# Kernel tuning notes

Measured on AMD Instinct MI355X. Metric: run time of the kernel, lower is better.

Reference implementation:

```python
import jax, jax.numpy as jnp
import numpy as np

N_NODES = 100000
N_EDGES = 1600000


def gcn_conv(x, edge_index, W, b):
    # PyG GCNConv: add self-loops, symmetric degree normalization,
    # linear transform, scatter-sum aggregation, + bias.
    n = x.shape[0]
    loop = jnp.arange(n, dtype=edge_index.dtype)
    src = jnp.concatenate([edge_index[0], loop])
    dst = jnp.concatenate([edge_index[1], loop])
    deg = jnp.zeros((n,), x.dtype).at[dst].add(1.0)
    dinv = jnp.where(deg > 0, deg ** -0.5, 0.0)
    norm = dinv[src] * dinv[dst]            # [E+N]
    h = x @ W                               # [N, out]
    msg = h[src] * norm[:, None]            # gather + scale
    out = jax.ops.segment_sum(msg, dst, num_segments=n)
    return out + b


def setup_inputs() -> dict:
    key = jax.random.key(0)
    k1, k2, k3, k4 = jax.random.split(key, 4)
    d_in, d_lat, d_out = 512, 128, 64
    x = jax.random.normal(k1, (N_NODES, d_in), jnp.float32)
    edge_index = jax.random.randint(k2, (2, N_EDGES), 0, N_NODES, jnp.int64)
    W1 = jax.random.normal(k3, (d_in, d_lat), jnp.float32) * (d_in ** -0.5)
    b1 = jnp.zeros((d_lat,), jnp.float32)
    W2 = jax.random.normal(k4, (d_lat, d_out), jnp.float32) * (d_lat ** -0.5)
    b2 = jnp.zeros((d_out,), jnp.float32)
    return {"x": x, "edge_index": edge_index, "W1": W1, "b1": b1, "W2": W2, "b2": b2}


def reference(x, edge_index, W1, b1, W2, b2):
    h = gcn_conv(x, edge_index, W1, b1)
    h = gcn_conv(h, edge_index, W2, b2)
    return jax.nn.relu(h)
```

## Files before the change

kernel.cpp:

```cpp
#include <hip/hip_runtime.h>
#include <hip/hip_bf16.h>

typedef unsigned short u16;
typedef unsigned int   u32;

#define N_NODES 100000
#define N_EDGES 1600000

__device__ __forceinline__ float bf2f(u16 u) {
    union { u32 i; float f; } c; c.i = ((u32)u) << 16; return c.f;
}
__device__ __forceinline__ u16 f2bf(float f) {
    union { float f; u32 i; } c; c.f = f;
    u32 u = c.i;
    u += 0x7fffu + ((u >> 16) & 1u);
    return (u16)(u >> 16);
}
__device__ __forceinline__ void acc4(uint2 d, float& a0, float& a1, float& a2, float& a3) {
    a0 += bf2f((u16)(d.x & 0xffffu));
    a1 += bf2f((u16)(d.x >> 16));
    a2 += bf2f((u16)(d.y & 0xffffu));
    a3 += bf2f((u16)(d.y >> 16));
}

__global__ void k_detect(const u32* __restrict__ ei, int* __restrict__ flag) {
    if (threadIdx.x == 0 && blockIdx.x == 0) {
        u32 h = ei[1] | ei[3] | ei[5] | ei[7];
        *flag = (h == 0u) ? 1 : 0;
    }
}
__device__ __forceinline__ int edge_at(const u32* ei, int f, long pos) {
    return f ? (int)ei[2 * pos] : (int)ei[pos];
}


__global__ void k_degree(const u32* __restrict__ ei, const int* __restrict__ flag,
                         int* __restrict__ deg) {
    int e4 = blockIdx.x * 256 + threadIdx.x;
    int f = *flag;
    long e = 4L * e4;
    if (e + 3 < N_EDGES) {
        int d0, d1, d2, d3;
        if (f) {
            uint4 a = *(const uint4*)&ei[2 * ((long)N_EDGES + e)];
            uint4 b = *(const uint4*)&ei[2 * ((long)N_EDGES + e) + 4];
            d0 = (int)a.x; d1 = (int)a.z; d2 = (int)b.x; d3 = (int)b.z;
        } else {
            uint4 a = *(const uint4*)&ei[(long)N_EDGES + e];
            d0 = (int)a.x; d1 = (int)a.y; d2 = (int)a.z; d3 = (int)a.w;
        }
        atomicAdd(&deg[d0], 1); atomicAdd(&deg[d1], 1);
        atomicAdd(&deg[d2], 1); atomicAdd(&deg[d3], 1);
    } else {
        for (; e < N_EDGES; e++) atomicAdd(&deg[edge_at(ei, f, (long)N_EDGES + e)], 1);
    }
}

__global__ void k_scan_part(const int* __restrict__ deg, int* __restrict__ rowstart,
                            int* __restrict__ bsums) {
    __shared__ int sh[256];
    const int t = threadIdx.x, b = blockIdx.x;
    const int base = b * 2048 + t * 8;
    int v[8]; int s = 0;
#pragma unroll
    for (int i = 0; i < 8; i++) {
        int idx = base + i;
        v[i] = (idx < N_NODES) ? deg[idx] : 0;
        s += v[i];
    }
    sh[t] = s;
    __syncthreads();
    for (int d = 1; d < 256; d <<= 1) {
        int x = (t >= d) ? sh[t - d] : 0;
        __syncthreads();
        sh[t] += x;
        __syncthreads();
    }
    int acc = sh[t] - s;
#pragma unroll
    for (int i = 0; i < 8; i++) {
        int idx = base + i;
        if (idx < N_NODES) rowstart[idx] = acc;
        acc += v[i];
    }
    if (t == 255) bsums[b] = sh[255];
}

__global__ void k_scan_sums(const int* __restrict__ bsums, int* __restrict__ boffs, int nb) {
    if (threadIdx.x == 0 && blockIdx.x == 0) {
        int r = 0;
        for (int i = 0; i < nb; i++) { boffs[i] = r; r += bsums[i]; }
    }
}

__global__ void k_scan_add_dinv(int* __restrict__ rowstart, const int* __restrict__ boffs,
                                const int* __restrict__ deg, float* __restrict__ dinv,
                                int* __restrict__ cursor) {
    int i = blockIdx.x * blockDim.x + threadIdx.x;
    if (i < N_NODES) {
        int r = rowstart[i] + boffs[i >> 11];
        rowstart[i] = r;
        cursor[i] = r;
        dinv[i] = rsqrtf((float)(deg[i] + 1));
    }
    if (i == 0) rowstart[N_NODES] = N_EDGES;
}

__global__ void k_fill(const u32* __restrict__ ei, const int* __restrict__ flag,
                       int* __restrict__ cursor, int* __restrict__ csr) {
    int e4 = blockIdx.x * 256 + threadIdx.x;
    int f = *flag;
    long e = 4L * e4;
    if (e + 3 < N_EDGES) {
        int s0, s1, s2, s3, d0, d1, d2, d3;
        if (f) {
            uint4 a = *(const uint4*)&ei[2 * e];
            uint4 b = *(const uint4*)&ei[2 * e + 4];
            s0 = (int)a.x; s1 = (int)a.z; s2 = (int)b.x; s3 = (int)b.z;
            uint4 c = *(const uint4*)&ei[2 * ((long)N_EDGES + e)];
            uint4 d = *(const uint4*)&ei[2 * ((long)N_EDGES + e) + 4];
            d0 = (int)c.x; d1 = (int)c.z; d2 = (int)d.x; d3 = (int)d.z;
        } else {
            uint4 a = *(const uint4*)&ei[e];
            s0 = (int)a.x; s1 = (int)a.y; s2 = (int)a.z; s3 = (int)a.w;
            uint4 c = *(const uint4*)&ei[(long)N_EDGES + e];
            d0 = (int)c.x; d1 = (int)c.y; d2 = (int)c.z; d3 = (int)c.w;
        }
        csr[atomicAdd(&cursor[d0], 1)] = s0;
        csr[atomicAdd(&cursor[d1], 1)] = s1;
        csr[atomicAdd(&cursor[d2], 1)] = s2;
        csr[atomicAdd(&cursor[d3], 1)] = s3;
    } else {
        for (; e < N_EDGES; e++) {
            int s = edge_at(ei, f, e);
            int d = edge_at(ei, f, (long)N_EDGES + e);
            csr[atomicAdd(&cursor[d], 1)] = s;
        }
    }
}


__global__ void k_w12(const float* __restrict__ W1, const float* __restrict__ W2,
                      float* __restrict__ W12f) {
    int idx = blockIdx.x * 256 + threadIdx.x;
    int k = idx >> 6, n = idx & 63;
    float acc = 0.f;
#pragma unroll 4
    for (int j = 0; j < 128; j++) acc += W1[k * 128 + j] * W2[j * 64 + n];
    W12f[idx] = acc;
}

__global__ void k_c1(const float* __restrict__ b1, const float* __restrict__ W2,
                     float* __restrict__ c1) {
    int n = threadIdx.x;
    float acc = 0.f;
    for (int j = 0; j < 128; j++) acc += b1[j] * W2[j * 64 + n];
    c1[n] = acc;
}

__global__ void k_fragB(const float* __restrict__ W12f, u16* __restrict__ Bt) {
    int idx = blockIdx.x * 256 + threadIdx.x;
    int l = idx & 63, c = (idx >> 6) & 3, kt = idx >> 8;
    int n = c * 16 + (l & 15);
    int k0 = kt * 32 + (l >> 4) * 8;
    u32 p[4];
#pragma unroll
    for (int j = 0; j < 4; j++) {
        u16 a = f2bf(W12f[(k0 + 2 * j) * 64 + n]);
        u16 b = f2bf(W12f[(k0 + 2 * j + 1) * 64 + n]);
        p[j] = (u32)a | ((u32)b << 16);
    }
    *(uint4*)&Bt[(long)idx * 8] = make_uint4(p[0], p[1], p[2], p[3]);
}


__global__ __launch_bounds__(256) void gemm_x(const float* __restrict__ A,
                                              const u16* __restrict__ Bt,
                                              const float* __restrict__ dinv,
                                              u16* __restrict__ C, int M) {
    constexpr int SA = 40;
    __shared__ u16 As[128 * SA];
    typedef __attribute__((ext_vector_type(8))) short v8s;
    typedef __attribute__((ext_vector_type(4))) float v4f;

    const int t = threadIdx.x;
    const int wave = t >> 6, lane = t & 63;
    const int m = lane & 15, quad = lane >> 4;
    const int row0 = blockIdx.x * 128;

    v4f acc[2][4];
#pragma unroll
    for (int i = 0; i < 2; i++)
#pragma unroll
        for (int c = 0; c < 4; c++)
#pragma unroll
            for (int r = 0; r < 4; r++) acc[i][c][r] = 0.0f;

    const int arow = t >> 1, ahalf = t & 1;
    const long aoff = (long)(row0 + arow) * 512;
    const bool arow_ok = (row0 + arow) < M;

    for (int kt = 0; kt < 16; ++kt) {
        const int kk0 = kt * 32 + ahalf * 16;
        float4 f0 = make_float4(0.f, 0.f, 0.f, 0.f), f1 = f0, f2 = f0, f3 = f0;
        if (arow_ok) {
            f0 = *(const float4*)&A[aoff + kk0];
            f1 = *(const float4*)&A[aoff + kk0 + 4];
            f2 = *(const float4*)&A[aoff + kk0 + 8];
            f3 = *(const float4*)&A[aoff + kk0 + 12];
        }
        uint4 w0, w1;
        w0.x = (u32)f2bf(f0.x) | ((u32)f2bf(f0.y) << 16);
        w0.y = (u32)f2bf(f0.z) | ((u32)f2bf(f0.w) << 16);
        w0.z = (u32)f2bf(f1.x) | ((u32)f2bf(f1.y) << 16);
        w0.w = (u32)f2bf(f1.z) | ((u32)f2bf(f1.w) << 16);
        w1.x = (u32)f2bf(f2.x) | ((u32)f2bf(f2.y) << 16);
        w1.y = (u32)f2bf(f2.z) | ((u32)f2bf(f2.w) << 16);
        w1.z = (u32)f2bf(f3.x) | ((u32)f2bf(f3.y) << 16);
        w1.w = (u32)f2bf(f3.z) | ((u32)f2bf(f3.w) << 16);
        *(uint4*)&As[arow * SA + ahalf * 16] = w0;
        *(uint4*)&As[arow * SA + ahalf * 16 + 8] = w1;
        __syncthreads();
        v8s a0 = *(const v8s*)&As[(wave * 32 + m) * SA + quad * 8];
        v8s a1 = *(const v8s*)&As[(wave * 32 + 16 + m) * SA + quad * 8];
#pragma unroll
        for (int c = 0; c < 4; c++) {
            v8s b = *(const v8s*)&Bt[(long)((kt * 4 + c) * 64 + lane) * 8];
            acc[0][c] = __builtin_amdgcn_mfma_f32_16x16x32_bf16(a0, b, acc[0][c], 0, 0, 0);
            acc[1][c] = __builtin_amdgcn_mfma_f32_16x16x32_bf16(a1, b, acc[1][c], 0, 0, 0);
        }
        __syncthreads();
    }
#pragma unroll
    for (int i = 0; i < 2; i++)
#pragma unroll
        for (int r = 0; r < 4; r++) {
            int grow = row0 + wave * 32 + i * 16 + quad * 4 + r;
            if (grow < M) {
                float w = dinv[grow];
#pragma unroll
                for (int c = 0; c < 4; c++)
                    C[(long)grow * 64 + c * 16 + m] = f2bf(acc[i][c][r] * w);
            }
        }
}


__global__ __launch_bounds__(256) void agg_a(const u16* __restrict__ zp,
                                             const float* __restrict__ dinv,
                                             const int* __restrict__ rowstart,
                                             const int* __restrict__ csr,
                                             u16* __restrict__ yp,
                                             float* __restrict__ sfac) {
    const int wave = threadIdx.x >> 6, lane = threadIdx.x & 63;
    const int n = blockIdx.x * 4 + wave;
    const int g = lane >> 4, l = lane & 15;
    const uint2* z2 = (const uint2*)zp;
    float a0 = 0.f, a1 = 0.f, a2 = 0.f, a3 = 0.f, sd = 0.f;
    const float w0 = dinv[n];
    if (g == 0) {
        uint2 d = z2[(long)n * 16 + l];
        acc4(d, a0, a1, a2, a3);
        sd = w0;
    }
    const int i1 = rowstart[n + 1];
    int i = rowstart[n] + g;
    for (; i + 4 < i1; i += 8) {
        int s0 = csr[i], s1 = csr[i + 4];
        uint2 d0 = z2[(long)s0 * 16 + l];
        uint2 d1 = z2[(long)s1 * 16 + l];
        sd += dinv[s0] + dinv[s1];
        acc4(d0, a0, a1, a2, a3);
        acc4(d1, a0, a1, a2, a3);
    }
    if (i < i1) {
        int s = csr[i];
        uint2 d = z2[(long)s * 16 + l];
        sd += dinv[s];
        acc4(d, a0, a1, a2, a3);
    }
    a0 += __shfl_xor(a0, 16); a0 += __shfl_xor(a0, 32);
    a1 += __shfl_xor(a1, 16); a1 += __shfl_xor(a1, 32);
    a2 += __shfl_xor(a2, 16); a2 += __shfl_xor(a2, 32);
    a3 += __shfl_xor(a3, 16); a3 += __shfl_xor(a3, 32);
    sd += __shfl_xor(sd, 16); sd += __shfl_xor(sd, 32);
    if (g == 0) {
        float w2 = w0 * w0;
        uint2 o;
        o.x = (u32)f2bf(a0 * w2) | ((u32)f2bf(a1 * w2) << 16);
        o.y = (u32)f2bf(a2 * w2) | ((u32)f2bf(a3 * w2) << 16);
        ((uint2*)yp)[(long)n * 16 + l] = o;
        if (l == 0) sfac[n] = w0 * sd;
    }
}


__global__ __launch_bounds__(256) void agg_b(const u16* __restrict__ yp,
                                             const float* __restrict__ dinv,
                                             const int* __restrict__ rowstart,
                                             const int* __restrict__ csr,
                                             const float* __restrict__ sfac,
                                             const float* __restrict__ c1,
                                             const float* __restrict__ b2,
                                             float* __restrict__ out) {
    const int wave = threadIdx.x >> 6, lane = threadIdx.x & 63;
    const int n = blockIdx.x * 4 + wave;
    const int g = lane >> 4, l = lane & 15;
    const uint2* y2 = (const uint2*)yp;
    float a0 = 0.f, a1 = 0.f, a2 = 0.f, a3 = 0.f;
    if (g == 0) {
        uint2 d = y2[(long)n * 16 + l];
        acc4(d, a0, a1, a2, a3);
    }
    const int i1 = rowstart[n + 1];
    int i = rowstart[n] + g;
    for (; i + 4 < i1; i += 8) {
        int s0 = csr[i], s1 = csr[i + 4];
        uint2 d0 = y2[(long)s0 * 16 + l];
        uint2 d1 = y2[(long)s1 * 16 + l];
        acc4(d0, a0, a1, a2, a3);
        acc4(d1, a0, a1, a2, a3);
    }
    if (i < i1) {
        uint2 d = y2[(long)csr[i] * 16 + l];
        acc4(d, a0, a1, a2, a3);
    }
    a0 += __shfl_xor(a0, 16); a0 += __shfl_xor(a0, 32);
    a1 += __shfl_xor(a1, 16); a1 += __shfl_xor(a1, 32);
    a2 += __shfl_xor(a2, 16); a2 += __shfl_xor(a2, 32);
    a3 += __shfl_xor(a3, 16); a3 += __shfl_xor(a3, 32);
    if (g == 0) {
        const float w0 = dinv[n];
        const float sn = sfac[n];
        float4 cv = ((const float4*)c1)[l];
        float4 bv = ((const float4*)b2)[l];
        float4 r;
        r.x = fmaxf(a0 * w0 + sn * cv.x + bv.x, 0.f);
        r.y = fmaxf(a1 * w0 + sn * cv.y + bv.y, 0.f);
        r.z = fmaxf(a2 * w0 + sn * cv.z + bv.z, 0.f);
        r.w = fmaxf(a3 * w0 + sn * cv.w + bv.w, 0.f);
        ((float4*)out)[(long)n * 16 + l] = r;
    }
}


extern "C" void kernel_launch(void* const* d_in, const int* in_sizes, int n_in,
                              void* d_out, int out_size, void* d_ws, size_t ws_size,
                              hipStream_t stream) {
    const float* x  = (const float*)d_in[0];
    const u32*   ei = (const u32*)d_in[1];
    const float* W1 = (const float*)d_in[2];
    const float* b1 = (const float*)d_in[3];
    const float* W2 = (const float*)d_in[4];
    const float* b2 = (const float*)d_in[5];
    float* out = (float*)d_out;

    char* ws = (char*)d_ws;
    size_t o = 0;
    auto alloc = [&](size_t bytes) -> char* {
        char* p = ws + o;
        o = (o + bytes + 255) & ~(size_t)255;
        return p;
    };
    int*   deg      = (int*)  alloc(N_NODES * 4);
    float* dinv     = (float*)alloc(N_NODES * 4);
    int*   rowstart = (int*)  alloc((N_NODES + 1) * 4);
    int*   cursor   = (int*)  alloc(N_NODES * 4);
    int*   bsums    = (int*)  alloc(64 * 4);
    int*   boffs    = (int*)  alloc(64 * 4);
    int*   eflag    = (int*)  alloc(256);
    float* W12f     = (float*)alloc(512 * 64 * 4);
    u16*   Bt       = (u16*)  alloc(512 * 64 * 2);
    float* c1       = (float*)alloc(64 * 4);
    float* sfac     = (float*)alloc(N_NODES * 4);
    int*   csr      = (int*)  alloc((size_t)N_EDGES * 4);
    u16*   z        = (u16*)  alloc((size_t)N_NODES * 64 * 2);
    u16*   y        = (u16*)  alloc((size_t)N_NODES * 64 * 2);
    (void)ws_size;

    hipMemsetAsync(deg, 0, N_NODES * 4, stream);

    const int NB = (N_NODES + 255) / 256;
    const int EB4 = (N_EDGES / 4 + 255) / 256;
    const int SCAN_BLKS = (N_NODES + 2047) / 2048;

    k_detect<<<1, 64, 0, stream>>>(ei, eflag);
    k_degree<<<EB4, 256, 0, stream>>>(ei, eflag, deg);
    k_scan_part<<<SCAN_BLKS, 256, 0, stream>>>(deg, rowstart, bsums);
    k_scan_sums<<<1, 64, 0, stream>>>(bsums, boffs, SCAN_BLKS);
    k_scan_add_dinv<<<NB, 256, 0, stream>>>(rowstart, boffs, deg, dinv, cursor);
    k_fill<<<EB4, 256, 0, stream>>>(ei, eflag, cursor, csr);

    k_w12<<<128, 256, 0, stream>>>(W1, W2, W12f);
    k_c1<<<1, 64, 0, stream>>>(b1, W2, c1);
    k_fragB<<<16, 256, 0, stream>>>(W12f, Bt);

    gemm_x<<<(N_NODES + 127) / 128, 256, 0, stream>>>(x, Bt, dinv, z, N_NODES);
    agg_a<<<N_NODES / 4, 256, 0, stream>>>(z, dinv, rowstart, csr, y, sfac);
    agg_b<<<N_NODES / 4, 256, 0, stream>>>(y, dinv, rowstart, csr, sfac, c1, b2, out);
}
```

Before: 615.5 us.

## Convert edges to int32, slice atomics by node range, widen aggregation loads

Adds a conversion pass that packs the int64 edge list into int32 src/dst arrays. Degree counting and CSR fill now run in 8 groups of blocks, each owning one destination node slice, so each group's atomics touch a cache-sized range of nodes. Every group re-reads the full destination array, which multiplies that read traffic by eight. The aggregation kernels switch from 16 lanes of 8-byte loads to 8 lanes of 16-byte loads per row, processing 8 edges per wave step with a three-stage shuffle reduction.

```diff
diff --git a/kernel.cpp b/kernel.cpp
--- a/kernel.cpp
+++ b/kernel.cpp
@@ -6,6 +6,9 @@
 
 #define N_NODES 100000
 #define N_EDGES 1600000
+#define NQ      (N_EDGES / 4)
+#define SLICE   12500
+#define BPG     96
 
 __device__ __forceinline__ float bf2f(u16 u) {
     union { u32 i; float f; } c; c.i = ((u32)u) << 16; return c.f;
@@ -16,11 +19,11 @@
     u += 0x7fffu + ((u >> 16) & 1u);
     return (u16)(u >> 16);
 }
-__device__ __forceinline__ void acc4(uint2 d, float& a0, float& a1, float& a2, float& a3) {
-    a0 += bf2f((u16)(d.x & 0xffffu));
-    a1 += bf2f((u16)(d.x >> 16));
-    a2 += bf2f((u16)(d.y & 0xffffu));
-    a3 += bf2f((u16)(d.y >> 16));
+__device__ __forceinline__ void acc8(uint4 d, float* a) {
+    a[0] += bf2f((u16)(d.x & 0xffffu)); a[1] += bf2f((u16)(d.x >> 16));
+    a[2] += bf2f((u16)(d.y & 0xffffu)); a[3] += bf2f((u16)(d.y >> 16));
+    a[4] += bf2f((u16)(d.z & 0xffffu)); a[5] += bf2f((u16)(d.z >> 16));
+    a[6] += bf2f((u16)(d.w & 0xffffu)); a[7] += bf2f((u16)(d.w >> 16));
 }
 
 __global__ void k_detect(const u32* __restrict__ ei, int* __restrict__ flag) {
@@ -29,30 +32,35 @@
         *flag = (h == 0u) ? 1 : 0;
     }
 }
-__device__ __forceinline__ int edge_at(const u32* ei, int f, long pos) {
-    return f ? (int)ei[2 * pos] : (int)ei[pos];
-}
-
-
-__global__ void k_degree(const u32* __restrict__ ei, const int* __restrict__ flag,
-                         int* __restrict__ deg) {
-    int e4 = blockIdx.x * 256 + threadIdx.x;
-    int f = *flag;
-    long e = 4L * e4;
-    if (e + 3 < N_EDGES) {
-        int d0, d1, d2, d3;
-        if (f) {
-            uint4 a = *(const uint4*)&ei[2 * ((long)N_EDGES + e)];
-            uint4 b = *(const uint4*)&ei[2 * ((long)N_EDGES + e) + 4];
-            d0 = (int)a.x; d1 = (int)a.z; d2 = (int)b.x; d3 = (int)b.z;
-        } else {
-            uint4 a = *(const uint4*)&ei[(long)N_EDGES + e];
-            d0 = (int)a.x; d1 = (int)a.y; d2 = (int)a.z; d3 = (int)a.w;
-        }
-        atomicAdd(&deg[d0], 1); atomicAdd(&deg[d1], 1);
-        atomicAdd(&deg[d2], 1); atomicAdd(&deg[d3], 1);
+
+__global__ __launch_bounds__(256) void k_convert(const u32* __restrict__ ei,
+                                                 const int* __restrict__ flag,
+                                                 uint4* __restrict__ src4,
+                                                 uint4* __restrict__ dst4) {
+    int q = blockIdx.x * 256 + threadIdx.x;
+    if (q >= NQ) return;
+    const uint4* e4 = (const uint4*)ei;
+    if (*flag) {
+        uint4 a = e4[2 * q],          b = e4[2 * q + 1];
+        src4[q] = make_uint4(a.x, a.z, b.x, b.z);
+        uint4 c = e4[2 * NQ + 2 * q], d = e4[2 * NQ + 2 * q + 1];
+        dst4[q] = make_uint4(c.x, c.z, d.x, d.z);
     } else {
-        for (; e < N_EDGES; e++) atomicAdd(&deg[edge_at(ei, f, (long)N_EDGES + e)], 1);
+        src4[q] = e4[q];
+        dst4[q] = e4[NQ + q];
+    }
+}
+
+__global__ __launch_bounds__(256) void k_degree(const uint4* __restrict__ dst4,
+                                                int* __restrict__ deg) {
+    const int g = blockIdx.x & 7, bb = blockIdx.x >> 3;
+    const int lo = g * SLICE, hi = lo + SLICE;
+    for (int q = bb * 256 + threadIdx.x; q < NQ; q += BPG * 256) {
+        uint4 d = dst4[q];
+        if ((int)d.x >= lo && (int)d.x < hi) atomicAdd(&deg[d.x], 1);
+        if ((int)d.y >= lo && (int)d.y < hi) atomicAdd(&deg[d.y], 1);
+        if ((int)d.z >= lo && (int)d.z < hi) atomicAdd(&deg[d.z], 1);
+        if ((int)d.w >= lo && (int)d.w < hi) atomicAdd(&deg[d.w], 1);
     }
 }
 
@@ -106,36 +114,18 @@
     if (i == 0) rowstart[N_NODES] = N_EDGES;
 }
 
-__global__ void k_fill(const u32* __restrict__ ei, const int* __restrict__ flag,
-                       int* __restrict__ cursor, int* __restrict__ csr) {
-    int e4 = blockIdx.x * 256 + threadIdx.x;
-    int f = *flag;
-    long e = 4L * e4;
-    if (e + 3 < N_EDGES) {
-        int s0, s1, s2, s3, d0, d1, d2, d3;
-        if (f) {
-            uint4 a = *(const uint4*)&ei[2 * e];
-            uint4 b = *(const uint4*)&ei[2 * e + 4];
-            s0 = (int)a.x; s1 = (int)a.z; s2 = (int)b.x; s3 = (int)b.z;
-            uint4 c = *(const uint4*)&ei[2 * ((long)N_EDGES + e)];
-            uint4 d = *(const uint4*)&ei[2 * ((long)N_EDGES + e) + 4];
-            d0 = (int)c.x; d1 = (int)c.z; d2 = (int)d.x; d3 = (int)d.z;
-        } else {
-            uint4 a = *(const uint4*)&ei[e];
-            s0 = (int)a.x; s1 = (int)a.y; s2 = (int)a.z; s3 = (int)a.w;
-            uint4 c = *(const uint4*)&ei[(long)N_EDGES + e];
-            d0 = (int)c.x; d1 = (int)c.y; d2 = (int)c.z; d3 = (int)c.w;
-        }
-        csr[atomicAdd(&cursor[d0], 1)] = s0;
-        csr[atomicAdd(&cursor[d1], 1)] = s1;
-        csr[atomicAdd(&cursor[d2], 1)] = s2;
-        csr[atomicAdd(&cursor[d3], 1)] = s3;
-    } else {
-        for (; e < N_EDGES; e++) {
-            int s = edge_at(ei, f, e);
-            int d = edge_at(ei, f, (long)N_EDGES + e);
-            csr[atomicAdd(&cursor[d], 1)] = s;
-        }
+__global__ __launch_bounds__(256) void k_fill(const uint4* __restrict__ dst4,
+                                              const int* __restrict__ src32,
+                                              int* __restrict__ cursor,
+                                              int* __restrict__ csr) {
+    const int g = blockIdx.x & 7, bb = blockIdx.x >> 3;
+    const int lo = g * SLICE, hi = lo + SLICE;
+    for (int q = bb * 256 + threadIdx.x; q < NQ; q += BPG * 256) {
+        uint4 d = dst4[q];
+        if ((int)d.x >= lo && (int)d.x < hi) csr[atomicAdd(&cursor[d.x], 1)] = src32[4 * q];
+        if ((int)d.y >= lo && (int)d.y < hi) csr[atomicAdd(&cursor[d.y], 1)] = src32[4 * q + 1];
+        if ((int)d.z >= lo && (int)d.z < hi) csr[atomicAdd(&cursor[d.z], 1)] = src32[4 * q + 2];
+        if ((int)d.w >= lo && (int)d.w < hi) csr[atomicAdd(&cursor[d.w], 1)] = src32[4 * q + 3];
     }
 }
 
@@ -254,42 +244,45 @@
                                              float* __restrict__ sfac) {
     const int wave = threadIdx.x >> 6, lane = threadIdx.x & 63;
     const int n = blockIdx.x * 4 + wave;
-    const int g = lane >> 4, l = lane & 15;
-    const uint2* z2 = (const uint2*)zp;
-    float a0 = 0.f, a1 = 0.f, a2 = 0.f, a3 = 0.f, sd = 0.f;
+    const int g = lane >> 3, l = lane & 7;
+    const uint4* z4 = (const uint4*)zp;
+    float a[8] = {0.f, 0.f, 0.f, 0.f, 0.f, 0.f, 0.f, 0.f};
+    float sd = 0.f;
     const float w0 = dinv[n];
     if (g == 0) {
-        uint2 d = z2[(long)n * 16 + l];
-        acc4(d, a0, a1, a2, a3);
+        acc8(z4[(long)n * 8 + l], a);
         sd = w0;
     }
     const int i1 = rowstart[n + 1];
     int i = rowstart[n] + g;
-    for (; i + 4 < i1; i += 8) {
-        int s0 = csr[i], s1 = csr[i + 4];
-        uint2 d0 = z2[(long)s0 * 16 + l];
-        uint2 d1 = z2[(long)s1 * 16 + l];
+    for (; i + 8 < i1; i += 16) {
+        int s0 = csr[i], s1 = csr[i + 8];
+        uint4 d0 = z4[(long)s0 * 8 + l];
+        uint4 d1 = z4[(long)s1 * 8 + l];
         sd += dinv[s0] + dinv[s1];
-        acc4(d0, a0, a1, a2, a3);
-        acc4(d1, a0, a1, a2, a3);
-    }
-    if (i < i1) {
+        acc8(d0, a); acc8(d1, a);
+    }
+    for (; i < i1; i += 8) {
         int s = csr[i];
-        uint2 d = z2[(long)s * 16 + l];
+        uint4 d = z4[(long)s * 8 + l];
         sd += dinv[s];
-        acc4(d, a0, a1, a2, a3);
-    }
-    a0 += __shfl_xor(a0, 16); a0 += __shfl_xor(a0, 32);
-    a1 += __shfl_xor(a1, 16); a1 += __shfl_xor(a1, 32);
-    a2 += __shfl_xor(a2, 16); a2 += __shfl_xor(a2, 32);
-    a3 += __shfl_xor(a3, 16); a3 += __shfl_xor(a3, 32);
-    sd += __shfl_xor(sd, 16); sd += __shfl_xor(sd, 32);
+        acc8(d, a);
+    }
+#pragma unroll
+    for (int j = 0; j < 8; j++) {
+        a[j] += __shfl_xor(a[j], 8);
+        a[j] += __shfl_xor(a[j], 16);
+        a[j] += __shfl_xor(a[j], 32);
+    }
+    sd += __shfl_xor(sd, 8); sd += __shfl_xor(sd, 16); sd += __shfl_xor(sd, 32);
     if (g == 0) {
         float w2 = w0 * w0;
-        uint2 o;
-        o.x = (u32)f2bf(a0 * w2) | ((u32)f2bf(a1 * w2) << 16);
-        o.y = (u32)f2bf(a2 * w2) | ((u32)f2bf(a3 * w2) << 16);
-        ((uint2*)yp)[(long)n * 16 + l] = o;
+        uint4 o;
+        o.x = (u32)f2bf(a[0] * w2) | ((u32)f2bf(a[1] * w2) << 16);
+        o.y = (u32)f2bf(a[2] * w2) | ((u32)f2bf(a[3] * w2) << 16);
+        o.z = (u32)f2bf(a[4] * w2) | ((u32)f2bf(a[5] * w2) << 16);
+        o.w = (u32)f2bf(a[6] * w2) | ((u32)f2bf(a[7] * w2) << 16);
+        ((uint4*)yp)[(long)n * 8 + l] = o;
         if (l == 0) sfac[n] = w0 * sd;
     }
 }
@@ -305,41 +298,44 @@
                                              float* __restrict__ out) {
     const int wave = threadIdx.x >> 6, lane = threadIdx.x & 63;
     const int n = blockIdx.x * 4 + wave;
-    const int g = lane >> 4, l = lane & 15;
-    const uint2* y2 = (const uint2*)yp;
-    float a0 = 0.f, a1 = 0.f, a2 = 0.f, a3 = 0.f;
-    if (g == 0) {
-        uint2 d = y2[(long)n * 16 + l];
-        acc4(d, a0, a1, a2, a3);
-    }
+    const int g = lane >> 3, l = lane & 7;
+    const uint4* y4 = (const uint4*)yp;
+    float a[8] = {0.f, 0.f, 0.f, 0.f, 0.f, 0.f, 0.f, 0.f};
+    if (g == 0) acc8(y4[(long)n * 8 + l], a);
     const int i1 = rowstart[n + 1];
     int i = rowstart[n] + g;
-    for (; i + 4 < i1; i += 8) {
-        int s0 = csr[i], s1 = csr[i + 4];
-        uint2 d0 = y2[(long)s0 * 16 + l];
-        uint2 d1 = y2[(long)s1 * 16 + l];
-        acc4(d0, a0, a1, a2, a3);
-        acc4(d1, a0, a1, a2, a3);
-    }
-    if (i < i1) {
-        uint2 d = y2[(long)csr[i] * 16 + l];
-        acc4(d, a0, a1, a2, a3);
-    }
-    a0 += __shfl_xor(a0, 16); a0 += __shfl_xor(a0, 32);
-    a1 += __shfl_xor(a1, 16); a1 += __shfl_xor(a1, 32);
-    a2 += __shfl_xor(a2, 16); a2 += __shfl_xor(a2, 32);
-    a3 += __shfl_xor(a3, 16); a3 += __shfl_xor(a3, 32);
+    for (; i + 8 < i1; i += 16) {
+        int s0 = csr[i], s1 = csr[i + 8];
+        uint4 d0 = y4[(long)s0 * 8 + l];
+        uint4 d1 = y4[(long)s1 * 8 + l];
+        acc8(d0, a); acc8(d1, a);
+    }
+    for (; i < i1; i += 8) {
+        uint4 d = y4[(long)csr[i] * 8 + l];
+        acc8(d, a);
+    }
+#pragma unroll
+    for (int j = 0; j < 8; j++) {
+        a[j] += __shfl_xor(a[j], 8);
+        a[j] += __shfl_xor(a[j], 16);
+        a[j] += __shfl_xor(a[j], 32);
+    }
     if (g == 0) {
         const float w0 = dinv[n];
         const float sn = sfac[n];
-        float4 cv = ((const float4*)c1)[l];
-        float4 bv = ((const float4*)b2)[l];
-        float4 r;
-        r.x = fmaxf(a0 * w0 + sn * cv.x + bv.x, 0.f);
-        r.y = fmaxf(a1 * w0 + sn * cv.y + bv.y, 0.f);
-        r.z = fmaxf(a2 * w0 + sn * cv.z + bv.z, 0.f);
-        r.w = fmaxf(a3 * w0 + sn * cv.w + bv.w, 0.f);
-        ((float4*)out)[(long)n * 16 + l] = r;
+        float4 c0 = ((const float4*)c1)[2 * l], c4 = ((const float4*)c1)[2 * l + 1];
+        float4 b0 = ((const float4*)b2)[2 * l], b4 = ((const float4*)b2)[2 * l + 1];
+        float4 r0, r1;
+        r0.x = fmaxf(a[0] * w0 + sn * c0.x + b0.x, 0.f);
+        r0.y = fmaxf(a[1] * w0 + sn * c0.y + b0.y, 0.f);
+        r0.z = fmaxf(a[2] * w0 + sn * c0.z + b0.z, 0.f);
+        r0.w = fmaxf(a[3] * w0 + sn * c0.w + b0.w, 0.f);
+        r1.x = fmaxf(a[4] * w0 + sn * c4.x + b4.x, 0.f);
+        r1.y = fmaxf(a[5] * w0 + sn * c4.y + b4.y, 0.f);
+        r1.z = fmaxf(a[6] * w0 + sn * c4.z + b4.z, 0.f);
+        r1.w = fmaxf(a[7] * w0 + sn * c4.w + b4.w, 0.f);
+        ((float4*)out)[(long)n * 16 + 2 * l]     = r0;
+        ((float4*)out)[(long)n * 16 + 2 * l + 1] = r1;
     }
 }
 
@@ -373,6 +369,8 @@
     u16*   Bt       = (u16*)  alloc(512 * 64 * 2);
     float* c1       = (float*)alloc(64 * 4);
     float* sfac     = (float*)alloc(N_NODES * 4);
+    uint4* src4     = (uint4*)alloc((size_t)N_EDGES * 4);
+    uint4* dst4     = (uint4*)alloc((size_t)N_EDGES * 4);
     int*   csr      = (int*)  alloc((size_t)N_EDGES * 4);
     u16*   z        = (u16*)  alloc((size_t)N_NODES * 64 * 2);
     u16*   y        = (u16*)  alloc((size_t)N_NODES * 64 * 2);
@@ -381,15 +379,16 @@
     hipMemsetAsync(deg, 0, N_NODES * 4, stream);
 
     const int NB = (N_NODES + 255) / 256;
-    const int EB4 = (N_EDGES / 4 + 255) / 256;
+    const int CQ = (NQ + 255) / 256;
     const int SCAN_BLKS = (N_NODES + 2047) / 2048;
 
     k_detect<<<1, 64, 0, stream>>>(ei, eflag);
-    k_degree<<<EB4, 256, 0, stream>>>(ei, eflag, deg);
+    k_convert<<<CQ, 256, 0, stream>>>(ei, eflag, src4, dst4);
+    k_degree<<<8 * BPG, 256, 0, stream>>>(dst4, deg);
     k_scan_part<<<SCAN_BLKS, 256, 0, stream>>>(deg, rowstart, bsums);
     k_scan_sums<<<1, 64, 0, stream>>>(bsums, boffs, SCAN_BLKS);
     k_scan_add_dinv<<<NB, 256, 0, stream>>>(rowstart, boffs, deg, dinv, cursor);
-    k_fill<<<EB4, 256, 0, stream>>>(ei, eflag, cursor, csr);
+    k_fill<<<8 * BPG, 256, 0, stream>>>(dst4, (const int*)src4, cursor, csr);
 
     k_w12<<<128, 256, 0, stream>>>(W1, W2, W12f);
     k_c1<<<1, 64, 0, stream>>>(b1, W2, c1);
```

Result: faster. 571.4 us (-7.2%).
